# Kernel optimization log

Hardware: AMD Instinct MI355X
Metric: run time of the kernel (lower is better)

Reference implementation:

```python
import jax, jax.numpy as jnp
import numpy as np

B, S, DIN, DOUT = 32, 4096, 1024, 1024

def setup_inputs() -> dict:
    key = jax.random.key(0)
    k1, k2, k3, k4 = jax.random.split(key, 4)
    return {
        "input": jax.random.normal(k1, (B, DIN), dtype=jnp.float32),
        "source_hids": jax.random.normal(k2, (B, S, DOUT), dtype=jnp.float32),
        "seg_scores": jax.random.uniform(k3, (B, S), dtype=jnp.float32),
        "W": jax.random.normal(k4, (DOUT, DIN), dtype=jnp.float32) * 0.1,
    }

def reference(input, source_hids, seg_scores, W):
    # x = input @ W^T : [B, Dout]
    x = jnp.einsum('bi,oi->bo', input, W)
    # scores: broadcast dot over feature dim -> [B, S]
    attn_scores = jnp.einsum('bsd,bd->bs', source_hids, x)
    attn_scores = attn_scores - 100.0 * (1.0 - seg_scores)
    attn_scores = jax.nn.softmax(attn_scores, axis=1)
    # context vector: weighted sum over source positions -> [B, Dout]
    ctx = jnp.einsum('bs,bsd->bd', attn_scores, source_hids)
    return (ctx, attn_scores)
```

## Files before the change

kernel.cpp:

```cpp
#include <hip/hip_runtime.h>
#include <math.h>

#define BB 32
#define SS 4096
#define DIN 1024
#define DOUT 1024
#define NCHUNK 32
#define ROWS_PER_BLOCK (SS / NCHUNK)
#define ROWS_PER_WAVE (ROWS_PER_BLOCK / 4)
#define PART_STRIDE 1040
#define THR 25.0f

typedef float vf4 __attribute__((ext_vector_type(4)));

__device__ inline vf4 ntload4(const float* p) {
  return __builtin_nontemporal_load((const vf4*)p);
}

__global__ __launch_bounds__(256) void proj_kernel(const float* __restrict__ input,
                                                   const float* __restrict__ W,
                                                   float* __restrict__ x) {
  const int b = blockIdx.x >> 5;
  const int ochunk = blockIdx.x & 31;
  __shared__ float inp[DIN];
  const int t = threadIdx.x;
  ((vf4*)inp)[t] = ((const vf4*)(input + (size_t)b * DIN))[t];
  __syncthreads();
  const int wave = t >> 6, lane = t & 63;
#pragma unroll
  for (int j = 0; j < 8; ++j) {
    const int o = ochunk * 32 + wave * 8 + j;
    const vf4* wrow = (const vf4*)(W + (size_t)o * DIN);
    vf4 prod = (vf4)0.f;
#pragma unroll
    for (int k = 0; k < 4; ++k) prod += wrow[lane + 64 * k] * ((const vf4*)inp)[lane + 64 * k];
    float sum = prod.x + prod.y + prod.z + prod.w;
#pragma unroll
    for (int off = 32; off; off >>= 1) sum += __shfl_down(sum, off);
    if (lane == 0) x[(size_t)b * DOUT + o] = sum;
  }
}

__global__ __launch_bounds__(256) void pass_kernel(const float* __restrict__ hids,
                                                   const float* __restrict__ seg,
                                                   const float* __restrict__ x,
                                                   float* __restrict__ raw_scores,
                                                   float* __restrict__ partials) {
  const int b = blockIdx.x >> 5;
  const int chunk = blockIdx.x & 31;
  const int t = threadIdx.x;
  __shared__ float xs[DOUT];
  __shared__ float buf[4][DOUT];
  __shared__ float sbuf[ROWS_PER_BLOCK];
  __shared__ float wstat[8];
  ((vf4*)xs)[t] = ((const vf4*)(x + (size_t)b * DOUT))[t];
  __syncthreads();
  const int wave = t >> 6, lane = t & 63;
  vf4 xv[4];
#pragma unroll
  for (int k = 0; k < 4; ++k) xv[k] = ((const vf4*)xs)[lane + 64 * k];

  const int s0 = chunk * ROWS_PER_BLOCK + wave * ROWS_PER_WAVE;
  const float* base = hids + ((size_t)b * SS + s0) * (size_t)DOUT;
  const float* segb = seg + (size_t)b * SS + s0;

  const float segv = segb[lane & 31];

  vf4 h[4];
#pragma unroll
  for (int k = 0; k < 4; ++k) h[k] = ntload4(base + (lane + 64 * k) * 4);

  vf4 hn[4];
#pragma unroll
  for (int k = 0; k < 4; ++k) hn[k] = ntload4(base + DOUT + (lane + 64 * k) * 4);

  vf4 prod0 = h[0] * xv[0] + h[1] * xv[1] + h[2] * xv[2] + h[3] * xv[3];
  float dot0 = prod0.x + prod0.y + prod0.z + prod0.w;
#pragma unroll
  for (int off = 32; off; off >>= 1) dot0 += __shfl_xor(dot0, off);
  float M = dot0 - 100.f * (1.f - __shfl(segv, 0));
  if (lane == 0) sbuf[wave * ROWS_PER_WAVE] = M;
  float l = 1.f;
  vf4 acc[4];
#pragma unroll
  for (int k = 0; k < 4; ++k) { acc[k] = h[k]; h[k] = hn[k]; }

#pragma unroll 4
  for (int r = 1; r < ROWS_PER_WAVE; ++r) {
    if (r + 1 < ROWS_PER_WAVE) {
      const float* nb = base + (size_t)(r + 1) * DOUT;
#pragma unroll
      for (int k = 0; k < 4; ++k) hn[k] = ntload4(nb + (lane + 64 * k) * 4);
    }

    vf4 prod = h[0] * xv[0] + h[1] * xv[1] + h[2] * xv[2] + h[3] * xv[3];
    float dot = prod.x + prod.y + prod.z + prod.w;
#pragma unroll
    for (int off = 32; off; off >>= 1) dot += __shfl_xor(dot, off);

    const float score = dot - 100.f * (1.f - __shfl(segv, r));
    if (lane == 0) sbuf[wave * ROWS_PER_WAVE + r] = score;

    float p;
    if (__builtin_expect(score > M + THR, 0)) {
      const float corr = __expf(M - score);
      l *= corr;
#pragma unroll
      for (int k = 0; k < 4; ++k) acc[k] *= corr;
      M = score;
      p = 1.f;
    } else {
      p = __expf(score - M);
    }
    l += p;
#pragma unroll
    for (int k = 0; k < 4; ++k) acc[k] += p * h[k];
#pragma unroll
    for (int k = 0; k < 4; ++k) h[k] = hn[k];
  }

  if (lane == 0) { wstat[wave] = M; wstat[4 + wave] = l; }
  __syncthreads();
  const float mb = fmaxf(fmaxf(wstat[0], wstat[1]), fmaxf(wstat[2], wstat[3]));
  const float scale = __expf(M - mb);
#pragma unroll
  for (int k = 0; k < 4; ++k)
    ((vf4*)buf[wave])[lane + 64 * k] = acc[k] * scale;
  __syncthreads();

  if (t < ROWS_PER_BLOCK)
    raw_scores[(size_t)b * SS + chunk * ROWS_PER_BLOCK + t] = sbuf[t];

  float* part = partials + ((size_t)b * NCHUNK + chunk) * PART_STRIDE;
  vf4 v0 = ((const vf4*)buf[0])[t];
  vf4 v1 = ((const vf4*)buf[1])[t];
  vf4 v2 = ((const vf4*)buf[2])[t];
  vf4 v3 = ((const vf4*)buf[3])[t];
  ((vf4*)(part + 16))[t] = (v0 + v1) + (v2 + v3);
  if (t == 0) {
    const float lb = wstat[4] * __expf(wstat[0] - mb) + wstat[5] * __expf(wstat[1] - mb) +
                     wstat[6] * __expf(wstat[2] - mb) + wstat[7] * __expf(wstat[3] - mb);
    part[0] = mb;
    part[1] = lb;
  }
}

__global__ __launch_bounds__(128) void combine_kernel(const float* __restrict__ partials,
                                                      float* __restrict__ out_ctx,
                                                      float* __restrict__ out_attn) {
  const int b = blockIdx.x >> 3;
  const int part = blockIdx.x & 7;
  const int t = threadIdx.x;
  const float* pb = partials + (size_t)b * NCHUNK * PART_STRIDE;

  __shared__ float sm[NCHUNK], sl[NCHUNK];
  if (t < NCHUNK) {
    sm[t] = pb[(size_t)t * PART_STRIDE];
    sl[t] = pb[(size_t)t * PART_STRIDE + 1];
  }
  __syncthreads();

  float m = -INFINITY;
#pragma unroll
  for (int j = 0; j < NCHUNK; ++j) m = fmaxf(m, sm[j]);
  float l = 0.f;
#pragma unroll
  for (int j = 0; j < NCHUNK; ++j) l += sl[j] * __expf(sm[j] - m);
  const float inv_l = 1.f / l;

  float c = 0.f;
#pragma unroll 8
  for (int j = 0; j < NCHUNK; ++j)
    c += __expf(sm[j] - m) * pb[(size_t)j * PART_STRIDE + 16 + part * 128 + t];
  out_ctx[(size_t)b * DOUT + part * 128 + t] = c * inv_l;

  float* arow = out_attn + (size_t)b * SS + part * 512;
  float4 v = ((float4*)arow)[t];
  v.x = __expf(v.x - m) * inv_l;
  v.y = __expf(v.y - m) * inv_l;
  v.z = __expf(v.z - m) * inv_l;
  v.w = __expf(v.w - m) * inv_l;
  ((float4*)arow)[t] = v;
}

extern "C" void kernel_launch(void* const* d_in, const int* in_sizes, int n_in,
                              void* d_out, int out_size, void* d_ws, size_t ws_size,
                              hipStream_t stream) {
  const float* input = (const float*)d_in[0];
  const float* hids  = (const float*)d_in[1];
  const float* seg   = (const float*)d_in[2];
  const float* W     = (const float*)d_in[3];
  float* out = (float*)d_out;
  float* out_ctx  = out;
  float* out_attn = out + (size_t)BB * DOUT;

  float* x        = (float*)d_ws;
  float* partials = x + (size_t)BB * DOUT;

  proj_kernel<<<BB * 32, 256, 0, stream>>>(input, W, x);
  pass_kernel<<<BB * NCHUNK, 256, 0, stream>>>(hids, seg, x, out_attn, partials);
  combine_kernel<<<BB * 8, 128, 0, stream>>>(partials, out_ctx, out_attn);
}
```

Before: 104.1 us.

## Fuse combine into pass kernel via last-block atomic and process two rows per iteration

Removes the separate combine kernel launch: each pass block increments a per-batch atomic counter, and the last block to finish does the cross-chunk softmax merge, writes ctx and normalizes the attention row. The counter is zeroed in the projection kernel. The main loop now processes two source rows per iteration with a deeper prefetch, so two dot-product reductions interleave. This adds threadfences, an atomic, and a serialized tail done by one block per batch, plus higher register pressure.

```diff
diff --git a/kernel.cpp b/kernel.cpp
--- a/kernel.cpp
+++ b/kernel.cpp
@@ -19,11 +19,13 @@
 
 __global__ __launch_bounds__(256) void proj_kernel(const float* __restrict__ input,
                                                    const float* __restrict__ W,
-                                                   float* __restrict__ x) {
+                                                   float* __restrict__ x,
+                                                   int* __restrict__ cnt) {
   const int b = blockIdx.x >> 5;
   const int ochunk = blockIdx.x & 31;
   __shared__ float inp[DIN];
   const int t = threadIdx.x;
+  if (blockIdx.x == 0 && t < BB) cnt[t] = 0;
   ((vf4*)inp)[t] = ((const vf4*)(input + (size_t)b * DIN))[t];
   __syncthreads();
   const int wave = t >> 6, lane = t & 63;
@@ -45,7 +47,9 @@
                                                    const float* __restrict__ seg,
                                                    const float* __restrict__ x,
                                                    float* __restrict__ raw_scores,
-                                                   float* __restrict__ partials) {
+                                                   float* __restrict__ out_ctx,
+                                                   float* __restrict__ partials,
+                                                   int* __restrict__ cnt) {
   const int b = blockIdx.x >> 5;
   const int chunk = blockIdx.x & 31;
   const int t = threadIdx.x;
@@ -53,6 +57,8 @@
   __shared__ float buf[4][DOUT];
   __shared__ float sbuf[ROWS_PER_BLOCK];
   __shared__ float wstat[8];
+  __shared__ float sm[NCHUNK], sl[NCHUNK];
+  __shared__ int isLast;
   ((vf4*)xs)[t] = ((const vf4*)(x + (size_t)b * DOUT))[t];
   __syncthreads();
   const int wave = t >> 6, lane = t & 63;
@@ -66,57 +72,95 @@
 
   const float segv = segb[lane & 31];
 
-  vf4 h[4];
-#pragma unroll
-  for (int k = 0; k < 4; ++k) h[k] = ntload4(base + (lane + 64 * k) * 4);
-
-  vf4 hn[4];
-#pragma unroll
-  for (int k = 0; k < 4; ++k) hn[k] = ntload4(base + DOUT + (lane + 64 * k) * 4);
-
-  vf4 prod0 = h[0] * xv[0] + h[1] * xv[1] + h[2] * xv[2] + h[3] * xv[3];
+  vf4 h0[4], h1[4], n0[4], n1[4];
+#pragma unroll
+  for (int k = 0; k < 4; ++k) h0[k] = ntload4(base + (lane + 64 * k) * 4);
+#pragma unroll
+  for (int k = 0; k < 4; ++k) h1[k] = ntload4(base + DOUT + (lane + 64 * k) * 4);
+#pragma unroll
+  for (int k = 0; k < 4; ++k) n0[k] = ntload4(base + 2 * DOUT + (lane + 64 * k) * 4);
+#pragma unroll
+  for (int k = 0; k < 4; ++k) n1[k] = ntload4(base + 3 * DOUT + (lane + 64 * k) * 4);
+
+  vf4 prod0 = h0[0] * xv[0] + h0[1] * xv[1] + h0[2] * xv[2] + h0[3] * xv[3];
   float dot0 = prod0.x + prod0.y + prod0.z + prod0.w;
-#pragma unroll
-  for (int off = 32; off; off >>= 1) dot0 += __shfl_xor(dot0, off);
+  vf4 prod1 = h1[0] * xv[0] + h1[1] * xv[1] + h1[2] * xv[2] + h1[3] * xv[3];
+  float dot1 = prod1.x + prod1.y + prod1.z + prod1.w;
+#pragma unroll
+  for (int off = 32; off; off >>= 1) { dot0 += __shfl_xor(dot0, off); dot1 += __shfl_xor(dot1, off); }
+
   float M = dot0 - 100.f * (1.f - __shfl(segv, 0));
-  if (lane == 0) sbuf[wave * ROWS_PER_WAVE] = M;
   float l = 1.f;
   vf4 acc[4];
 #pragma unroll
-  for (int k = 0; k < 4; ++k) { acc[k] = h[k]; h[k] = hn[k]; }
-
-#pragma unroll 4
-  for (int r = 1; r < ROWS_PER_WAVE; ++r) {
-    if (r + 1 < ROWS_PER_WAVE) {
-      const float* nb = base + (size_t)(r + 1) * DOUT;
-#pragma unroll
-      for (int k = 0; k < 4; ++k) hn[k] = ntload4(nb + (lane + 64 * k) * 4);
-    }
-
-    vf4 prod = h[0] * xv[0] + h[1] * xv[1] + h[2] * xv[2] + h[3] * xv[3];
-    float dot = prod.x + prod.y + prod.z + prod.w;
-#pragma unroll
-    for (int off = 32; off; off >>= 1) dot += __shfl_xor(dot, off);
-
-    const float score = dot - 100.f * (1.f - __shfl(segv, r));
-    if (lane == 0) sbuf[wave * ROWS_PER_WAVE + r] = score;
-
+  for (int k = 0; k < 4; ++k) acc[k] = h0[k];
+  if (lane == 0) sbuf[wave * ROWS_PER_WAVE] = M;
+
+  {
+    const float score = dot1 - 100.f * (1.f - __shfl(segv, 1));
+    if (lane == 0) sbuf[wave * ROWS_PER_WAVE + 1] = score;
     float p;
     if (__builtin_expect(score > M + THR, 0)) {
       const float corr = __expf(M - score);
       l *= corr;
 #pragma unroll
       for (int k = 0; k < 4; ++k) acc[k] *= corr;
-      M = score;
-      p = 1.f;
-    } else {
-      p = __expf(score - M);
-    }
+      M = score; p = 1.f;
+    } else p = __expf(score - M);
     l += p;
 #pragma unroll
-    for (int k = 0; k < 4; ++k) acc[k] += p * h[k];
-#pragma unroll
-    for (int k = 0; k < 4; ++k) h[k] = hn[k];
+    for (int k = 0; k < 4; ++k) acc[k] += p * h1[k];
+  }
+
+#pragma unroll 2
+  for (int rr = 1; rr < ROWS_PER_WAVE / 2; ++rr) {
+#pragma unroll
+    for (int k = 0; k < 4; ++k) { h0[k] = n0[k]; h1[k] = n1[k]; }
+    if (rr + 1 < ROWS_PER_WAVE / 2) {
+      const float* pb0 = base + (size_t)(2 * rr + 2) * DOUT;
+      const float* pb1 = base + (size_t)(2 * rr + 3) * DOUT;
+#pragma unroll
+      for (int k = 0; k < 4; ++k) n0[k] = ntload4(pb0 + (lane + 64 * k) * 4);
+#pragma unroll
+      for (int k = 0; k < 4; ++k) n1[k] = ntload4(pb1 + (lane + 64 * k) * 4);
+    }
+
+    vf4 pa = h0[0] * xv[0] + h0[1] * xv[1] + h0[2] * xv[2] + h0[3] * xv[3];
+    vf4 pbv = h1[0] * xv[0] + h1[1] * xv[1] + h1[2] * xv[2] + h1[3] * xv[3];
+    float da = pa.x + pa.y + pa.z + pa.w;
+    float db = pbv.x + pbv.y + pbv.z + pbv.w;
+#pragma unroll
+    for (int off = 32; off; off >>= 1) { da += __shfl_xor(da, off); db += __shfl_xor(db, off); }
+
+    const float sa = da - 100.f * (1.f - __shfl(segv, 2 * rr));
+    const float sb = db - 100.f * (1.f - __shfl(segv, 2 * rr + 1));
+    if (lane == 0) {
+      sbuf[wave * ROWS_PER_WAVE + 2 * rr] = sa;
+      sbuf[wave * ROWS_PER_WAVE + 2 * rr + 1] = sb;
+    }
+
+    float p;
+    if (__builtin_expect(sa > M + THR, 0)) {
+      const float corr = __expf(M - sa);
+      l *= corr;
+#pragma unroll
+      for (int k = 0; k < 4; ++k) acc[k] *= corr;
+      M = sa; p = 1.f;
+    } else p = __expf(sa - M);
+    l += p;
+#pragma unroll
+    for (int k = 0; k < 4; ++k) acc[k] += p * h0[k];
+
+    if (__builtin_expect(sb > M + THR, 0)) {
+      const float corr = __expf(M - sb);
+      l *= corr;
+#pragma unroll
+      for (int k = 0; k < 4; ++k) acc[k] *= corr;
+      M = sb; p = 1.f;
+    } else p = __expf(sb - M);
+    l += p;
+#pragma unroll
+    for (int k = 0; k < 4; ++k) acc[k] += p * h1[k];
   }
 
   if (lane == 0) { wstat[wave] = M; wstat[4 + wave] = l; }
@@ -143,44 +187,43 @@
     part[0] = mb;
     part[1] = lb;
   }
-}
-
-__global__ __launch_bounds__(128) void combine_kernel(const float* __restrict__ partials,
-                                                      float* __restrict__ out_ctx,
-                                                      float* __restrict__ out_attn) {
-  const int b = blockIdx.x >> 3;
-  const int part = blockIdx.x & 7;
-  const int t = threadIdx.x;
-  const float* pb = partials + (size_t)b * NCHUNK * PART_STRIDE;
-
-  __shared__ float sm[NCHUNK], sl[NCHUNK];
-  if (t < NCHUNK) {
-    sm[t] = pb[(size_t)t * PART_STRIDE];
-    sl[t] = pb[(size_t)t * PART_STRIDE + 1];
-  }
-  __syncthreads();
-
-  float m = -INFINITY;
-#pragma unroll
-  for (int j = 0; j < NCHUNK; ++j) m = fmaxf(m, sm[j]);
-  float l = 0.f;
-#pragma unroll
-  for (int j = 0; j < NCHUNK; ++j) l += sl[j] * __expf(sm[j] - m);
-  const float inv_l = 1.f / l;
-
-  float c = 0.f;
+
+  __threadfence();
+  if (t == 0) isLast = (atomicAdd(&cnt[b], 1) == NCHUNK - 1);
+  __syncthreads();
+  if (isLast) {
+    __threadfence();
+    const float* pball = partials + (size_t)b * NCHUNK * PART_STRIDE;
+    if (t < NCHUNK) {
+      sm[t] = pball[(size_t)t * PART_STRIDE];
+      sl[t] = pball[(size_t)t * PART_STRIDE + 1];
+    }
+    __syncthreads();
+    float m2 = -INFINITY;
+#pragma unroll
+    for (int j = 0; j < NCHUNK; ++j) m2 = fmaxf(m2, sm[j]);
+    float l2 = 0.f;
+#pragma unroll
+    for (int j = 0; j < NCHUNK; ++j) l2 += sl[j] * __expf(sm[j] - m2);
+    const float inv_l = 1.f / l2;
+
+    vf4 c = (vf4)0.f;
 #pragma unroll 8
-  for (int j = 0; j < NCHUNK; ++j)
-    c += __expf(sm[j] - m) * pb[(size_t)j * PART_STRIDE + 16 + part * 128 + t];
-  out_ctx[(size_t)b * DOUT + part * 128 + t] = c * inv_l;
-
-  float* arow = out_attn + (size_t)b * SS + part * 512;
-  float4 v = ((float4*)arow)[t];
-  v.x = __expf(v.x - m) * inv_l;
-  v.y = __expf(v.y - m) * inv_l;
-  v.z = __expf(v.z - m) * inv_l;
-  v.w = __expf(v.w - m) * inv_l;
-  ((float4*)arow)[t] = v;
+    for (int j = 0; j < NCHUNK; ++j)
+      c += __expf(sm[j] - m2) * ((const vf4*)(pball + (size_t)j * PART_STRIDE + 16))[t];
+    ((vf4*)(out_ctx + (size_t)b * DOUT))[t] = c * inv_l;
+
+    float* arow = raw_scores + (size_t)b * SS;
+#pragma unroll
+    for (int k = 0; k < 4; ++k) {
+      vf4 v = ((vf4*)arow)[t + 256 * k];
+      v.x = __expf(v.x - m2) * inv_l;
+      v.y = __expf(v.y - m2) * inv_l;
+      v.z = __expf(v.z - m2) * inv_l;
+      v.w = __expf(v.w - m2) * inv_l;
+      ((vf4*)arow)[t + 256 * k] = v;
+    }
+  }
 }
 
 extern "C" void kernel_launch(void* const* d_in, const int* in_sizes, int n_in,
@@ -196,8 +239,8 @@
 
   float* x        = (float*)d_ws;
   float* partials = x + (size_t)BB * DOUT;
-
-  proj_kernel<<<BB * 32, 256, 0, stream>>>(input, W, x);
-  pass_kernel<<<BB * NCHUNK, 256, 0, stream>>>(hids, seg, x, out_attn, partials);
-  combine_kernel<<<BB * 8, 128, 0, stream>>>(partials, out_ctx, out_attn);
-}
+  int*   cnt      = (int*)(partials + (size_t)BB * NCHUNK * PART_STRIDE);
+
+  proj_kernel<<<BB * 32, 256, 0, stream>>>(input, W, x, cnt);
+  pass_kernel<<<BB * NCHUNK, 256, 0, stream>>>(hids, seg, x, out_attn, out_ctx, partials, cnt);
+}
```

After: 376.1 us. +261.1%, slower.
